# Performance work log

Measured on AMD Instinct MI355X. Metric: run time of the kernel, lower is better.

The kernel has to match this reference:

```python
import jax, jax.numpy as jnp
import numpy as np

EMB = 1024
HEADS = 16
HEAD_DIM = EMB // HEADS
B, S = 4, 2048


def setup_inputs() -> dict:
    key = jax.random.key(0)
    ks = jax.random.split(key, 9)
    sc = 1.0 / np.sqrt(EMB)
    x = jax.random.normal(ks[0], (B, S, EMB), dtype=jnp.float32)
    Wq = jax.random.normal(ks[1], (EMB, EMB), dtype=jnp.float32) * sc
    bq = jax.random.normal(ks[2], (EMB,), dtype=jnp.float32) * 0.02
    Wk = jax.random.normal(ks[3], (EMB, EMB), dtype=jnp.float32) * sc
    bk = jax.random.normal(ks[4], (EMB,), dtype=jnp.float32) * 0.02
    Wv = jax.random.normal(ks[5], (EMB, EMB), dtype=jnp.float32) * sc
    bv = jax.random.normal(ks[6], (EMB,), dtype=jnp.float32) * 0.02
    Wo = jax.random.normal(ks[7], (EMB, EMB), dtype=jnp.float32) * sc
    bo = jax.random.normal(ks[8], (EMB,), dtype=jnp.float32) * 0.02
    # causal mask: 1 where allowed (lower triangular), 0 elsewhere
    causal_mask = jnp.tril(jnp.ones((S, S), dtype=jnp.int32))[None, None]
    return {"x": x, "Wq": Wq, "bq": bq, "Wk": Wk, "bk": bk,
            "Wv": Wv, "bv": bv, "Wo": Wo, "bo": bo,
            "causal_mask": causal_mask}


def reference(x, Wq, bq, Wk, bk, Wv, bv, Wo, bo, causal_mask):
    bs, seq, _ = x.shape
    # nn.Linear: x @ W.T + b; then view [bs, seq, H, hd] and transpose to [bs, H, seq, hd]
    def proj(W, b):
        return (x @ W.T + b).reshape(bs, seq, HEADS, HEAD_DIM).transpose(0, 2, 1, 3)
    q, k, v = proj(Wq, bq), proj(Wk, bk), proj(Wv, bv)
    scale = 1.0 / np.sqrt(HEAD_DIM).astype(np.float32)
    dots = jnp.einsum('bhqd,bhkd->bhqk', q, k) * scale  # [B, H, S, S]
    dots = jnp.where(causal_mask == 0, -jnp.inf, dots)
    attn = jax.nn.softmax(dots, axis=-1)
    out = jnp.einsum('bhqk,bhkd->bhqd', attn, v)  # [B, H, S, hd]
    out = out.transpose(0, 2, 1, 3).reshape(bs, seq, EMB)
    return out @ Wo.T + bo
```

## Files before the change

### kernel.cpp

```cpp
#include <hip/hip_runtime.h>
#include <hip/hip_bf16.h>

typedef __attribute__((ext_vector_type(8))) short short8;
typedef __attribute__((ext_vector_type(4))) float floatx4;

#define B_    4
#define S_    2048
#define EMB_  1024
#define NH_   16
#define HD_   64

#if __has_builtin(__builtin_amdgcn_exp2f)
#define EXP2F(x) __builtin_amdgcn_exp2f(x)
#else
#define EXP2F(x) exp2f(x)
#endif

__device__ __forceinline__ void async_cp16(const void* g, void* l) {
  __builtin_amdgcn_global_load_lds(
      (const __attribute__((address_space(1))) unsigned int*)g,
      (__attribute__((address_space(3))) unsigned int*)l, 16, 0, 0);
}

__device__ __forceinline__ ushort4 cvt4(const float4 f) {
  __bf16 t[4] = {(__bf16)f.x, (__bf16)f.y, (__bf16)f.z, (__bf16)f.w};
  return *(const ushort4*)t;
}

__global__ __launch_bounds__(256)
void cvt_kernel(const float* __restrict__ x,
                const float* __restrict__ wq, const float* __restrict__ wk,
                const float* __restrict__ wv, const float* __restrict__ wo,
                const float* __restrict__ bq, const float* __restrict__ bk,
                const float* __restrict__ bv,
                __bf16* __restrict__ xb, __bf16* __restrict__ Wcat,
                __bf16* __restrict__ Wob, float* __restrict__ bcat)
{
  const int NX4 = 2097152;
  const int NW4 = 262144;
  int g = blockIdx.x * 256 + threadIdx.x;
  if (g < NX4) {
    *(ushort4*)(xb + (size_t)g * 4) = cvt4(*(const float4*)(x + (size_t)g * 4));
    return;
  }
  g -= NX4;
  if (g < 3 * NW4) {
    const float* src = (g < NW4) ? wq : (g < 2 * NW4) ? wk : wv;
    const int gg = (g < NW4) ? g : (g < 2 * NW4) ? g - NW4 : g - 2 * NW4;
    *(ushort4*)(Wcat + (size_t)g * 4) = cvt4(*(const float4*)(src + (size_t)gg * 4));
    return;
  }
  g -= 3 * NW4;
  if (g < NW4) {
    *(ushort4*)(Wob + (size_t)g * 4) = cvt4(*(const float4*)(wo + (size_t)g * 4));
    return;
  }
  g -= NW4;
  if (g < 768) {
    const float* src = (g < 256) ? bq : (g < 512) ? bk : bv;
    *(float4*)(bcat + (size_t)g * 4) = *(const float4*)(src + (size_t)(g & 255) * 4);
  }
}

__global__ __launch_bounds__(256)
void gemm_qkv_kernel(const __bf16* __restrict__ A, const __bf16* __restrict__ W,
                     const float* __restrict__ bcat,
                     __bf16* __restrict__ Qb, __bf16* __restrict__ Kb,
                     __bf16* __restrict__ Vb)
{
  __shared__ __attribute__((aligned(16))) __bf16 As[128 * 32];
  __shared__ __attribute__((aligned(16))) __bf16 Ws[128 * 32];
  const int tid  = threadIdx.x;
  const int wave = tid >> 6, lane = tid & 63;
  const int l15  = lane & 15, quad = lane >> 4;
  const int wm   = wave >> 1, wn = wave & 1;
  const int bm   = blockIdx.y * 128;
  const int bn   = blockIdx.x * 128;
  const int widx = bn >> 10;
  const float QS = 0.180336880f;

  floatx4 acc[4][4];
#pragma unroll
  for (int i = 0; i < 4; ++i)
#pragma unroll
    for (int j = 0; j < 4; ++j) acc[i][j] = (floatx4){0.f, 0.f, 0.f, 0.f};

  const int srow = tid >> 2;
  const int scol = (tid & 3) << 3;
  const __bf16* Ag = A + (size_t)(bm + srow) * 1024 + scol;
  const __bf16* Wg = W + (size_t)(bn + srow) * 1024 + scol;
  __bf16* AsD = As + tid * 8;
  __bf16* WsD = Ws + tid * 8;

  for (int k0 = 0; k0 < 1024; k0 += 32) {
    __syncthreads();
    async_cp16(Ag + k0,             AsD);
    async_cp16(Ag + k0 + 64 * 1024, AsD + 2048);
    async_cp16(Wg + k0,             WsD);
    async_cp16(Wg + k0 + 64 * 1024, WsD + 2048);
    __syncthreads();
    short8 af[4], wf[4];
#pragma unroll
    for (int mi = 0; mi < 4; ++mi)
      af[mi] = *(const short8*)(As + ((wm * 64 + mi * 16 + l15) << 5) + (quad << 3));
#pragma unroll
    for (int ni = 0; ni < 4; ++ni)
      wf[ni] = *(const short8*)(Ws + ((wn * 64 + ni * 16 + l15) << 5) + (quad << 3));
#pragma unroll
    for (int mi = 0; mi < 4; ++mi)
#pragma unroll
      for (int ni = 0; ni < 4; ++ni)
        acc[mi][ni] = __builtin_amdgcn_mfma_f32_16x16x32_bf16(af[mi], wf[ni], acc[mi][ni], 0, 0, 0);
  }

#pragma unroll
  for (int ni = 0; ni < 4; ++ni) {
    const int n  = bn + wn * 64 + ni * 16 + l15;
    const float bvb = bcat[n];
    const int np = n & 1023;
    const int h = np >> 6, d = np & 63;
#pragma unroll
    for (int mi = 0; mi < 4; ++mi) {
      const int m0 = bm + wm * 64 + mi * 16 + quad * 4;
      const int b = m0 >> 11, s0 = m0 & 2047;
      floatx4 v = acc[mi][ni];
      if (widx == 0) {
        const size_t base = (size_t)(b * 16 + h) * (S_ * 64) + d;
#pragma unroll
        for (int r = 0; r < 4; ++r)
          Qb[base + (size_t)(s0 + r) * 64] = (__bf16)((v[r] + bvb) * QS);
      } else if (widx == 1) {
        const size_t base = (size_t)(b * 16 + h) * (S_ * 64) + d;
#pragma unroll
        for (int r = 0; r < 4; ++r)
          Kb[base + (size_t)(s0 + r) * 64] = (__bf16)(v[r] + bvb);
      } else {
        const size_t base = ((size_t)(b * 16 + h) * 64 + d) * S_ + s0;
        union { ushort4 u4; unsigned short u[4]; } pk;
#pragma unroll
        for (int r = 0; r < 4; ++r) {
          __bf16 hv = (__bf16)(v[r] + bvb);
          pk.u[r] = *(unsigned short*)&hv;
        }
        *(ushort4*)(Vb + base) = pk.u4;
      }
    }
  }
}

__global__ __launch_bounds__(256, 4)
void attn_kernel(__bf16* __restrict__ Q, const __bf16* __restrict__ K,
                 const __bf16* __restrict__ Vt)
{
  __shared__ __attribute__((aligned(16))) __bf16 Ks[64 * 72];
  __shared__ __attribute__((aligned(16))) __bf16 Vs[64 * 72];
  __shared__ __attribute__((aligned(16))) __bf16 Ps[4][16 * 72];

  const int tid  = threadIdx.x;
  const int wave = tid >> 6, lane = tid & 63;
  const int l15  = lane & 15, quad = lane >> 4;
  const int qtA  = blockIdx.x, bh = blockIdx.y;
  const size_t hb = (size_t)bh * (S_ * 64);
  const float MASKV = -1.0e30f;

  const int srow = tid >> 3;
  const int scol = (tid & 7) << 3;

  for (int qsel = 0; qsel < 2; ++qsel) {
    const int qt = qsel ? (31 - qtA) : qtA;
    const int qw = qt * 64 + wave * 16;
    const int myq = qw + l15;

    short8 aq[2];
#pragma unroll
    for (int kk = 0; kk < 2; ++kk)
      aq[kk] = *(const short8*)(Q + hb + (size_t)myq * 64 + kk * 32 + quad * 8);

    floatx4 oacc[4];
#pragma unroll
    for (int j = 0; j < 4; ++j) oacc[j] = (floatx4){0.f, 0.f, 0.f, 0.f};
    float lsum = 0.0f;
    float mrun = MASKV;

    uint4 kreg0, kreg1, vreg0, vreg1;
    {
      const __bf16* kp = K  + hb + (size_t)srow * 64 + scol;
      const __bf16* vp = Vt + hb + (size_t)srow * S_ + scol;
      kreg0 = *(const uint4*)kp;
      kreg1 = *(const uint4*)(kp + 32 * 64);
      vreg0 = *(const uint4*)vp;
      vreg1 = *(const uint4*)(vp + (size_t)32 * S_);
    }

    for (int kt = 0; kt <= qt; ++kt) {
      __syncthreads();
      *(uint4*)(&Ks[srow * 72 + scol])        = kreg0;
      *(uint4*)(&Ks[(srow + 32) * 72 + scol]) = kreg1;
      *(uint4*)(&Vs[srow * 72 + scol])        = vreg0;
      *(uint4*)(&Vs[(srow + 32) * 72 + scol]) = vreg1;
      __syncthreads();

      if (kt < qt) {
        const __bf16* kp = K  + hb + (size_t)((kt + 1) * 64 + srow) * 64 + scol;
        const __bf16* vp = Vt + hb + (size_t)srow * S_ + (kt + 1) * 64 + scol;
        kreg0 = *(const uint4*)kp;
        kreg1 = *(const uint4*)(kp + 32 * 64);
        vreg0 = *(const uint4*)vp;
        vreg1 = *(const uint4*)(vp + (size_t)32 * S_);
      }

      floatx4 sacc[4];
#pragma unroll
      for (int j = 0; j < 4; ++j) sacc[j] = (floatx4){0.f, 0.f, 0.f, 0.f};
#pragma unroll
      for (int kk = 0; kk < 2; ++kk) {
        short8 bk[4];
#pragma unroll
        for (int ni = 0; ni < 4; ++ni)
          bk[ni] = *(const short8*)(&Ks[(ni * 16 + l15) * 72 + kk * 32 + quad * 8]);
#pragma unroll
        for (int ni = 0; ni < 4; ++ni)
          sacc[ni] = __builtin_amdgcn_mfma_f32_16x16x32_bf16(bk[ni], aq[kk], sacc[ni], 0, 0, 0);
      }

      if (kt == qt) {
        const int kb = kt * 64 + quad * 4;
#pragma unroll
        for (int ni = 0; ni < 4; ++ni)
#pragma unroll
          for (int r = 0; r < 4; ++r)
            if (kb + ni * 16 + r > myq) sacc[ni][r] = MASKV;
      }

      float t0 = fmaxf(fmaxf(sacc[0][0], sacc[0][1]), fmaxf(sacc[0][2], sacc[0][3]));
      float t1 = fmaxf(fmaxf(sacc[1][0], sacc[1][1]), fmaxf(sacc[1][2], sacc[1][3]));
      float t2 = fmaxf(fmaxf(sacc[2][0], sacc[2][1]), fmaxf(sacc[2][2], sacc[2][3]));
      float t3 = fmaxf(fmaxf(sacc[3][0], sacc[3][1]), fmaxf(sacc[3][2], sacc[3][3]));
      float tmax = fmaxf(fmaxf(t0, t1), fmaxf(t2, t3));
      tmax = fmaxf(tmax, __shfl_xor(tmax, 16));
      tmax = fmaxf(tmax, __shfl_xor(tmax, 32));

      const float mold = mrun;
      const float mnew = fmaxf(mold, tmax);
      mrun = mnew;
      const float alpha = EXP2F(mold - mnew);

      float psum = 0.0f;
#pragma unroll
      for (int ni = 0; ni < 4; ++ni) {
        float4 p;
        p.x = EXP2F(sacc[ni][0] - mnew);
        p.y = EXP2F(sacc[ni][1] - mnew);
        p.z = EXP2F(sacc[ni][2] - mnew);
        p.w = EXP2F(sacc[ni][3] - mnew);
        psum += (p.x + p.y) + (p.z + p.w);
        *(ushort4*)(&Ps[wave][l15 * 72 + ni * 16 + quad * 4]) = cvt4(p);
      }
      lsum = lsum * alpha + psum;
#pragma unroll
      for (int ni = 0; ni < 4; ++ni)
#pragma unroll
        for (int r = 0; r < 4; ++r) oacc[ni][r] *= alpha;

      asm volatile("s_waitcnt lgkmcnt(0)" ::: "memory");
      __builtin_amdgcn_sched_barrier(0);

#pragma unroll
      for (int kk = 0; kk < 2; ++kk) {
        const short8 pf = *(const short8*)(&Ps[wave][l15 * 72 + kk * 32 + quad * 8]);
        short8 bv[4];
#pragma unroll
        for (int ni = 0; ni < 4; ++ni)
          bv[ni] = *(const short8*)(&Vs[(ni * 16 + l15) * 72 + kk * 32 + quad * 8]);
#pragma unroll
        for (int ni = 0; ni < 4; ++ni)
          oacc[ni] = __builtin_amdgcn_mfma_f32_16x16x32_bf16(bv[ni], pf, oacc[ni], 0, 0, 0);
      }
    }

    float l = lsum;
    l += __shfl_xor(l, 16);
    l += __shfl_xor(l, 32);
    const float inv = 1.0f / fmaxf(l, 1e-20f);
    const size_t rowb = hb + (size_t)myq * 64;
#pragma unroll
    for (int ni = 0; ni < 4; ++ni) {
      float4 o;
      o.x = oacc[ni][0] * inv;
      o.y = oacc[ni][1] * inv;
      o.z = oacc[ni][2] * inv;
      o.w = oacc[ni][3] * inv;
      *(ushort4*)(Q + rowb + ni * 16 + quad * 4) = cvt4(o);
    }
  }
}

__global__ __launch_bounds__(256)
void gemm_o_kernel(const __bf16* __restrict__ A, const __bf16* __restrict__ W,
                   const float* __restrict__ bias, float* __restrict__ out)
{
  __shared__ __attribute__((aligned(16))) __bf16 As[128 * 32];
  __shared__ __attribute__((aligned(16))) __bf16 Ws[128 * 32];
  const int tid  = threadIdx.x;
  const int wave = tid >> 6, lane = tid & 63;
  const int l15  = lane & 15, quad = lane >> 4;
  const int wm   = wave >> 1, wn = wave & 1;
  const int bm   = blockIdx.y * 128;
  const int bn   = blockIdx.x * 128;

  floatx4 acc[4][4];
#pragma unroll
  for (int i = 0; i < 4; ++i)
#pragma unroll
    for (int j = 0; j < 4; ++j) acc[i][j] = (floatx4){0.f, 0.f, 0.f, 0.f};

  const int srow = tid >> 2;
  const int scol = (tid & 3) << 3;
  const __bf16* Wg = W + (size_t)(bn + srow) * 1024 + scol;
  const int bb = bm >> 11;
  const int ss = (bm & 2047) + srow;
  __bf16* AsD = As + tid * 8;
  __bf16* WsD = Ws + tid * 8;

  for (int k0 = 0; k0 < 1024; k0 += 32) {
    const int c = k0 + scol, h = c >> 6, dd = c & 63;
    const __bf16* pa0 = A + (((size_t)(bb * 16 + h) * S_) + ss) * 64 + dd;
    __syncthreads();
    async_cp16(pa0,           AsD);
    async_cp16(pa0 + 64 * 64, AsD + 2048);
    async_cp16(Wg + k0,             WsD);
    async_cp16(Wg + k0 + 64 * 1024, WsD + 2048);
    __syncthreads();

    short8 af[4], wf[4];
#pragma unroll
    for (int mi = 0; mi < 4; ++mi)
      af[mi] = *(const short8*)(As + ((wm * 64 + mi * 16 + l15) << 5) + (quad << 3));
#pragma unroll
    for (int ni = 0; ni < 4; ++ni)
      wf[ni] = *(const short8*)(Ws + ((wn * 64 + ni * 16 + l15) << 5) + (quad << 3));
#pragma unroll
    for (int mi = 0; mi < 4; ++mi)
#pragma unroll
      for (int ni = 0; ni < 4; ++ni)
        acc[mi][ni] = __builtin_amdgcn_mfma_f32_16x16x32_bf16(af[mi], wf[ni], acc[mi][ni], 0, 0, 0);
  }

#pragma unroll
  for (int ni = 0; ni < 4; ++ni) {
    const int n = bn + wn * 64 + ni * 16 + l15;
    const float bvb = bias[n];
#pragma unroll
    for (int mi = 0; mi < 4; ++mi) {
      const int m0 = bm + wm * 64 + mi * 16 + quad * 4;
      floatx4 v = acc[mi][ni];
#pragma unroll
      for (int r = 0; r < 4; ++r)
        out[(size_t)(m0 + r) * 1024 + n] = v[r] + bvb;
    }
  }
}

extern "C" void kernel_launch(void* const* d_in, const int* in_sizes, int n_in,
                              void* d_out, int out_size, void* d_ws, size_t ws_size,
                              hipStream_t stream) {
  const float* x  = (const float*)d_in[0];
  const float* Wq = (const float*)d_in[1];
  const float* bq = (const float*)d_in[2];
  const float* Wk = (const float*)d_in[3];
  const float* bk = (const float*)d_in[4];
  const float* Wv = (const float*)d_in[5];
  const float* bv = (const float*)d_in[6];
  const float* Wo = (const float*)d_in[7];
  const float* bo = (const float*)d_in[8];

  const size_t BUF = (size_t)B_ * NH_ * S_ * HD_;
  __bf16* ws   = (__bf16*)d_ws;
  __bf16* xb   = ws;
  __bf16* Wcat = ws + 8388608;
  __bf16* Wob  = ws + 11534336;
  __bf16* Qb   = ws + 12582912;
  float*  bcat = (float*)(ws + 20971520);
  __bf16* Kb   = (__bf16*)d_out;
  __bf16* Vb   = (__bf16*)d_out + BUF;

  dim3 blk(256);
  cvt_kernel<<<12291, blk, 0, stream>>>(x, Wq, Wk, Wv, Wo, bq, bk, bv,
                                        xb, Wcat, Wob, bcat);
  gemm_qkv_kernel<<<dim3(24, 64), blk, 0, stream>>>(xb, Wcat, bcat, Qb, Kb, Vb);
  attn_kernel<<<dim3(16, 64), blk, 0, stream>>>(Qb, Kb, Vb);
  gemm_o_kernel<<<dim3(8, 64), blk, 0, stream>>>(Qb, Wob, bo, (float*)d_out);
}
```

Measured before the change: 291.0 us.

## Process both paired query tiles in one KV sweep with lazy softmax rescale

Merges the two sequential query-tile passes (qtA and 31-qtA) into a single loop over key/value tiles. Each loaded K/V tile in LDS now serves both query tiles, which halves the global loads and barriers spent on the shared prefix. Softmax rescaling is skipped unless the running max grows by more than a threshold, which saves exp and multiply work on most iterations. The cost is double the accumulator registers, with the occupancy hint lowered from 4 to 3 blocks, and a per-wave Ps buffer for each query tile.

```diff
diff --git a/kernel.cpp b/kernel.cpp
--- a/kernel.cpp
+++ b/kernel.cpp
@@ -148,13 +148,51 @@
   }
 }
 
-__global__ __launch_bounds__(256, 4)
+__device__ __forceinline__ void softmax_update(
+    floatx4* s, float& mrun, float& lsum, floatx4* oacc,
+    __bf16* psbase, const int l15, const int quad)
+{
+  float t0 = fmaxf(fmaxf(s[0][0], s[0][1]), fmaxf(s[0][2], s[0][3]));
+  float t1 = fmaxf(fmaxf(s[1][0], s[1][1]), fmaxf(s[1][2], s[1][3]));
+  float t2 = fmaxf(fmaxf(s[2][0], s[2][1]), fmaxf(s[2][2], s[2][3]));
+  float t3 = fmaxf(fmaxf(s[3][0], s[3][1]), fmaxf(s[3][2], s[3][3]));
+  float tmax = fmaxf(fmaxf(t0, t1), fmaxf(t2, t3));
+  tmax = fmaxf(tmax, __shfl_xor(tmax, 16));
+  tmax = fmaxf(tmax, __shfl_xor(tmax, 32));
+
+  const float mold = mrun;
+  if (!__all(tmax <= mold + 8.0f)) {
+    const float mnew = fmaxf(mold, tmax);
+    const float alpha = EXP2F(mold - mnew);
+#pragma unroll
+    for (int ni = 0; ni < 4; ++ni)
+#pragma unroll
+      for (int r = 0; r < 4; ++r) oacc[ni][r] *= alpha;
+    lsum *= alpha;
+    mrun = mnew;
+  }
+  const float m = mrun;
+  float psum = 0.f;
+#pragma unroll
+  for (int ni = 0; ni < 4; ++ni) {
+    float4 p;
+    p.x = EXP2F(s[ni][0] - m);
+    p.y = EXP2F(s[ni][1] - m);
+    p.z = EXP2F(s[ni][2] - m);
+    p.w = EXP2F(s[ni][3] - m);
+    psum += (p.x + p.y) + (p.z + p.w);
+    *(ushort4*)(psbase + l15 * 72 + ni * 16 + quad * 4) = cvt4(p);
+  }
+  lsum += psum;
+}
+
+__global__ __launch_bounds__(256, 3)
 void attn_kernel(__bf16* __restrict__ Q, const __bf16* __restrict__ K,
                  const __bf16* __restrict__ Vt)
 {
   __shared__ __attribute__((aligned(16))) __bf16 Ks[64 * 72];
   __shared__ __attribute__((aligned(16))) __bf16 Vs[64 * 72];
-  __shared__ __attribute__((aligned(16))) __bf16 Ps[4][16 * 72];
+  __shared__ __attribute__((aligned(16))) __bf16 Ps[4][2][16 * 72];
 
   const int tid  = threadIdx.x;
   const int wave = tid >> 6, lane = tid & 63;
@@ -166,130 +204,150 @@
   const int srow = tid >> 3;
   const int scol = (tid & 7) << 3;
 
-  for (int qsel = 0; qsel < 2; ++qsel) {
-    const int qt = qsel ? (31 - qtA) : qtA;
-    const int qw = qt * 64 + wave * 16;
-    const int myq = qw + l15;
-
-    short8 aq[2];
-#pragma unroll
-    for (int kk = 0; kk < 2; ++kk)
-      aq[kk] = *(const short8*)(Q + hb + (size_t)myq * 64 + kk * 32 + quad * 8);
-
-    floatx4 oacc[4];
-#pragma unroll
-    for (int j = 0; j < 4; ++j) oacc[j] = (floatx4){0.f, 0.f, 0.f, 0.f};
-    float lsum = 0.0f;
-    float mrun = MASKV;
-
-    uint4 kreg0, kreg1, vreg0, vreg1;
-    {
-      const __bf16* kp = K  + hb + (size_t)srow * 64 + scol;
-      const __bf16* vp = Vt + hb + (size_t)srow * S_ + scol;
+  const int qtS = qtA;
+  const int qtB = 31 - qtA;
+  const int myqS = qtS * 64 + wave * 16 + l15;
+  const int myqB = qtB * 64 + wave * 16 + l15;
+
+  short8 aqS[2], aqB[2];
+#pragma unroll
+  for (int kk = 0; kk < 2; ++kk) {
+    aqS[kk] = *(const short8*)(Q + hb + (size_t)myqS * 64 + kk * 32 + quad * 8);
+    aqB[kk] = *(const short8*)(Q + hb + (size_t)myqB * 64 + kk * 32 + quad * 8);
+  }
+
+  floatx4 oaccS[4], oaccB[4];
+#pragma unroll
+  for (int j = 0; j < 4; ++j) {
+    oaccS[j] = (floatx4){0.f, 0.f, 0.f, 0.f};
+    oaccB[j] = (floatx4){0.f, 0.f, 0.f, 0.f};
+  }
+  float lsumS = 0.f, lsumB = 0.f;
+  float mrunS = MASKV, mrunB = MASKV;
+
+  uint4 kreg0, kreg1, vreg0, vreg1;
+  {
+    const __bf16* kp = K  + hb + (size_t)srow * 64 + scol;
+    const __bf16* vp = Vt + hb + (size_t)srow * S_ + scol;
+    kreg0 = *(const uint4*)kp;
+    kreg1 = *(const uint4*)(kp + 32 * 64);
+    vreg0 = *(const uint4*)vp;
+    vreg1 = *(const uint4*)(vp + (size_t)32 * S_);
+  }
+
+  for (int kt = 0; kt <= qtB; ++kt) {
+    const bool haveS = (kt <= qtS);
+
+    __syncthreads();
+    *(uint4*)(&Ks[srow * 72 + scol])        = kreg0;
+    *(uint4*)(&Ks[(srow + 32) * 72 + scol]) = kreg1;
+    *(uint4*)(&Vs[srow * 72 + scol])        = vreg0;
+    *(uint4*)(&Vs[(srow + 32) * 72 + scol]) = vreg1;
+    __syncthreads();
+
+    if (kt < qtB) {
+      const __bf16* kp = K  + hb + (size_t)((kt + 1) * 64 + srow) * 64 + scol;
+      const __bf16* vp = Vt + hb + (size_t)srow * S_ + (kt + 1) * 64 + scol;
       kreg0 = *(const uint4*)kp;
       kreg1 = *(const uint4*)(kp + 32 * 64);
       vreg0 = *(const uint4*)vp;
       vreg1 = *(const uint4*)(vp + (size_t)32 * S_);
     }
 
-    for (int kt = 0; kt <= qt; ++kt) {
-      __syncthreads();
-      *(uint4*)(&Ks[srow * 72 + scol])        = kreg0;
-      *(uint4*)(&Ks[(srow + 32) * 72 + scol]) = kreg1;
-      *(uint4*)(&Vs[srow * 72 + scol])        = vreg0;
-      *(uint4*)(&Vs[(srow + 32) * 72 + scol]) = vreg1;
-      __syncthreads();
-
-      if (kt < qt) {
-        const __bf16* kp = K  + hb + (size_t)((kt + 1) * 64 + srow) * 64 + scol;
-        const __bf16* vp = Vt + hb + (size_t)srow * S_ + (kt + 1) * 64 + scol;
-        kreg0 = *(const uint4*)kp;
-        kreg1 = *(const uint4*)(kp + 32 * 64);
-        vreg0 = *(const uint4*)vp;
-        vreg1 = *(const uint4*)(vp + (size_t)32 * S_);
+    floatx4 sS[4], sB[4];
+#pragma unroll
+    for (int j = 0; j < 4; ++j) {
+      sS[j] = (floatx4){0.f, 0.f, 0.f, 0.f};
+      sB[j] = (floatx4){0.f, 0.f, 0.f, 0.f};
+    }
+#pragma unroll
+    for (int kk = 0; kk < 2; ++kk) {
+      short8 bk[4];
+#pragma unroll
+      for (int ni = 0; ni < 4; ++ni)
+        bk[ni] = *(const short8*)(&Ks[(ni * 16 + l15) * 72 + kk * 32 + quad * 8]);
+#pragma unroll
+      for (int ni = 0; ni < 4; ++ni)
+        sB[ni] = __builtin_amdgcn_mfma_f32_16x16x32_bf16(bk[ni], aqB[kk], sB[ni], 0, 0, 0);
+      if (haveS) {
+#pragma unroll
+        for (int ni = 0; ni < 4; ++ni)
+          sS[ni] = __builtin_amdgcn_mfma_f32_16x16x32_bf16(bk[ni], aqS[kk], sS[ni], 0, 0, 0);
       }
-
-      floatx4 sacc[4];
-#pragma unroll
-      for (int j = 0; j < 4; ++j) sacc[j] = (floatx4){0.f, 0.f, 0.f, 0.f};
-#pragma unroll
-      for (int kk = 0; kk < 2; ++kk) {
-        short8 bk[4];
+    }
+
+    if (kt == qtB) {
+      const int kb = kt * 64 + quad * 4;
+#pragma unroll
+      for (int ni = 0; ni < 4; ++ni)
+#pragma unroll
+        for (int r = 0; r < 4; ++r)
+          if (kb + ni * 16 + r > myqB) sB[ni][r] = MASKV;
+    }
+    if (haveS) {
+      if (kt == qtS) {
+        const int kb = kt * 64 + quad * 4;
 #pragma unroll
         for (int ni = 0; ni < 4; ++ni)
-          bk[ni] = *(const short8*)(&Ks[(ni * 16 + l15) * 72 + kk * 32 + quad * 8]);
+#pragma unroll
+          for (int r = 0; r < 4; ++r)
+            if (kb + ni * 16 + r > myqS) sS[ni][r] = MASKV;
+      }
+      softmax_update(sS, mrunS, lsumS, oaccS, &Ps[wave][0][0], l15, quad);
+    }
+    softmax_update(sB, mrunB, lsumB, oaccB, &Ps[wave][1][0], l15, quad);
+
+    asm volatile("s_waitcnt lgkmcnt(0)" ::: "memory");
+    __builtin_amdgcn_sched_barrier(0);
+
+#pragma unroll
+    for (int kk = 0; kk < 2; ++kk) {
+      short8 bv[4];
+#pragma unroll
+      for (int ni = 0; ni < 4; ++ni)
+        bv[ni] = *(const short8*)(&Vs[(ni * 16 + l15) * 72 + kk * 32 + quad * 8]);
+      const short8 pfB = *(const short8*)(&Ps[wave][1][l15 * 72 + kk * 32 + quad * 8]);
+#pragma unroll
+      for (int ni = 0; ni < 4; ++ni)
+        oaccB[ni] = __builtin_amdgcn_mfma_f32_16x16x32_bf16(bv[ni], pfB, oaccB[ni], 0, 0, 0);
+      if (haveS) {
+        const short8 pfS = *(const short8*)(&Ps[wave][0][l15 * 72 + kk * 32 + quad * 8]);
 #pragma unroll
         for (int ni = 0; ni < 4; ++ni)
-          sacc[ni] = __builtin_amdgcn_mfma_f32_16x16x32_bf16(bk[ni], aq[kk], sacc[ni], 0, 0, 0);
+          oaccS[ni] = __builtin_amdgcn_mfma_f32_16x16x32_bf16(bv[ni], pfS, oaccS[ni], 0, 0, 0);
       }
-
-      if (kt == qt) {
-        const int kb = kt * 64 + quad * 4;
-#pragma unroll
-        for (int ni = 0; ni < 4; ++ni)
-#pragma unroll
-          for (int r = 0; r < 4; ++r)
-            if (kb + ni * 16 + r > myq) sacc[ni][r] = MASKV;
-      }
-
-      float t0 = fmaxf(fmaxf(sacc[0][0], sacc[0][1]), fmaxf(sacc[0][2], sacc[0][3]));
-      float t1 = fmaxf(fmaxf(sacc[1][0], sacc[1][1]), fmaxf(sacc[1][2], sacc[1][3]));
-      float t2 = fmaxf(fmaxf(sacc[2][0], sacc[2][1]), fmaxf(sacc[2][2], sacc[2][3]));
-      float t3 = fmaxf(fmaxf(sacc[3][0], sacc[3][1]), fmaxf(sacc[3][2], sacc[3][3]));
-      float tmax = fmaxf(fmaxf(t0, t1), fmaxf(t2, t3));
-      tmax = fmaxf(tmax, __shfl_xor(tmax, 16));
-      tmax = fmaxf(tmax, __shfl_xor(tmax, 32));
-
-      const float mold = mrun;
-      const float mnew = fmaxf(mold, tmax);
-      mrun = mnew;
-      const float alpha = EXP2F(mold - mnew);
-
-      float psum = 0.0f;
-#pragma unroll
-      for (int ni = 0; ni < 4; ++ni) {
-        float4 p;
-        p.x = EXP2F(sacc[ni][0] - mnew);
-        p.y = EXP2F(sacc[ni][1] - mnew);
-        p.z = EXP2F(sacc[ni][2] - mnew);
-        p.w = EXP2F(sacc[ni][3] - mnew);
-        psum += (p.x + p.y) + (p.z + p.w);
-        *(ushort4*)(&Ps[wave][l15 * 72 + ni * 16 + quad * 4]) = cvt4(p);
-      }
-      lsum = lsum * alpha + psum;
-#pragma unroll
-      for (int ni = 0; ni < 4; ++ni)
-#pragma unroll
-        for (int r = 0; r < 4; ++r) oacc[ni][r] *= alpha;
-
-      asm volatile("s_waitcnt lgkmcnt(0)" ::: "memory");
-      __builtin_amdgcn_sched_barrier(0);
-
-#pragma unroll
-      for (int kk = 0; kk < 2; ++kk) {
-        const short8 pf = *(const short8*)(&Ps[wave][l15 * 72 + kk * 32 + quad * 8]);
-        short8 bv[4];
-#pragma unroll
-        for (int ni = 0; ni < 4; ++ni)
-          bv[ni] = *(const short8*)(&Vs[(ni * 16 + l15) * 72 + kk * 32 + quad * 8]);
-#pragma unroll
-        for (int ni = 0; ni < 4; ++ni)
-          oacc[ni] = __builtin_amdgcn_mfma_f32_16x16x32_bf16(bv[ni], pf, oacc[ni], 0, 0, 0);
-      }
-    }
-
-    float l = lsum;
+    }
+  }
+
+  {
+    float l = lsumS;
     l += __shfl_xor(l, 16);
     l += __shfl_xor(l, 32);
     const float inv = 1.0f / fmaxf(l, 1e-20f);
-    const size_t rowb = hb + (size_t)myq * 64;
+    const size_t rowb = hb + (size_t)myqS * 64;
 #pragma unroll
     for (int ni = 0; ni < 4; ++ni) {
       float4 o;
-      o.x = oacc[ni][0] * inv;
-      o.y = oacc[ni][1] * inv;
-      o.z = oacc[ni][2] * inv;
-      o.w = oacc[ni][3] * inv;
+      o.x = oaccS[ni][0] * inv;
+      o.y = oaccS[ni][1] * inv;
+      o.z = oaccS[ni][2] * inv;
+      o.w = oaccS[ni][3] * inv;
+      *(ushort4*)(Q + rowb + ni * 16 + quad * 4) = cvt4(o);
+    }
+  }
+  {
+    float l = lsumB;
+    l += __shfl_xor(l, 16);
+    l += __shfl_xor(l, 32);
+    const float inv = 1.0f / fmaxf(l, 1e-20f);
+    const size_t rowb = hb + (size_t)myqB * 64;
+#pragma unroll
+    for (int ni = 0; ni < 4; ++ni) {
+      float4 o;
+      o.x = oaccB[ni][0] * inv;
+      o.y = oaccB[ni][1] * inv;
+      o.z = oaccB[ni][2] * inv;
+      o.w = oaccB[ni][3] * inv;
       *(ushort4*)(Q + rowb + ni * 16 + quad * 4) = cvt4(o);
     }
   }
```

Result: no change. 287.2 us (-1.3%).

## Switch attention to 32x32x16 MFMA with two 32-row waves and lazy rescale

Applied to the files above, without the earlier changes.

The attention kernel now runs two waves of 32 query rows each (128 threads) and uses 32x32x16 bf16 MFMAs instead of 16x16x32, which reduces LDS fragment reads per FLOP and cross-lane reductions. The K/V staging is reworked so each thread loads four contiguous 16-byte chunks. The online-softmax rescale is skipped unless some lane's tile max exceeds the running max by more than 8 (in log2 units), which saves exp and multiply work per tile but lets unnormalised values grow by up to 2^8. Fewer threads per block may lower latency hiding, since each block now has half as many waves.

```diff
diff --git a/kernel.cpp b/kernel.cpp
--- a/kernel.cpp
+++ b/kernel.cpp
@@ -3,6 +3,7 @@
 
 typedef __attribute__((ext_vector_type(8))) short short8;
 typedef __attribute__((ext_vector_type(4))) float floatx4;
+typedef __attribute__((ext_vector_type(16))) float floatx16;
 
 #define B_    4
 #define S_    2048
@@ -148,150 +149,156 @@
   }
 }
 
-__global__ __launch_bounds__(256, 4)
+__global__ __launch_bounds__(128, 2)
 void attn_kernel(__bf16* __restrict__ Q, const __bf16* __restrict__ K,
                  const __bf16* __restrict__ Vt)
 {
   __shared__ __attribute__((aligned(16))) __bf16 Ks[64 * 72];
   __shared__ __attribute__((aligned(16))) __bf16 Vs[64 * 72];
-  __shared__ __attribute__((aligned(16))) __bf16 Ps[4][16 * 72];
+  __shared__ __attribute__((aligned(16))) __bf16 Ps[2][32 * 72];
 
   const int tid  = threadIdx.x;
   const int wave = tid >> 6, lane = tid & 63;
-  const int l15  = lane & 15, quad = lane >> 4;
+  const int l31  = lane & 31, h = lane >> 5;
   const int qtA  = blockIdx.x, bh = blockIdx.y;
   const size_t hb = (size_t)bh * (S_ * 64);
   const float MASKV = -1.0e30f;
 
-  const int srow = tid >> 3;
-  const int scol = (tid & 7) << 3;
+  const int srow = tid >> 1;
+  const int scol = (tid & 1) << 5;
 
   for (int qsel = 0; qsel < 2; ++qsel) {
     const int qt = qsel ? (31 - qtA) : qtA;
-    const int qw = qt * 64 + wave * 16;
-    const int myq = qw + l15;
-
-    short8 aq[2];
-#pragma unroll
-    for (int kk = 0; kk < 2; ++kk)
-      aq[kk] = *(const short8*)(Q + hb + (size_t)myq * 64 + kk * 32 + quad * 8);
-
-    floatx4 oacc[4];
-#pragma unroll
-    for (int j = 0; j < 4; ++j) oacc[j] = (floatx4){0.f, 0.f, 0.f, 0.f};
+    const int myq = qt * 64 + wave * 32 + l31;
+
+    short8 aq[4];
+#pragma unroll
+    for (int s = 0; s < 4; ++s)
+      aq[s] = *(const short8*)(Q + hb + (size_t)myq * 64 + s * 16 + h * 8);
+
+    floatx16 oacc[2];
+#pragma unroll
+    for (int dt = 0; dt < 2; ++dt)
+#pragma unroll
+      for (int r = 0; r < 16; ++r) oacc[dt][r] = 0.f;
     float lsum = 0.0f;
     float mrun = MASKV;
 
-    uint4 kreg0, kreg1, vreg0, vreg1;
+    uint4 kreg[4], vreg[4];
     {
       const __bf16* kp = K  + hb + (size_t)srow * 64 + scol;
       const __bf16* vp = Vt + hb + (size_t)srow * S_ + scol;
-      kreg0 = *(const uint4*)kp;
-      kreg1 = *(const uint4*)(kp + 32 * 64);
-      vreg0 = *(const uint4*)vp;
-      vreg1 = *(const uint4*)(vp + (size_t)32 * S_);
+#pragma unroll
+      for (int u = 0; u < 4; ++u) {
+        kreg[u] = *(const uint4*)(kp + u * 8);
+        vreg[u] = *(const uint4*)(vp + u * 8);
+      }
     }
 
     for (int kt = 0; kt <= qt; ++kt) {
       __syncthreads();
-      *(uint4*)(&Ks[srow * 72 + scol])        = kreg0;
-      *(uint4*)(&Ks[(srow + 32) * 72 + scol]) = kreg1;
-      *(uint4*)(&Vs[srow * 72 + scol])        = vreg0;
-      *(uint4*)(&Vs[(srow + 32) * 72 + scol]) = vreg1;
+#pragma unroll
+      for (int u = 0; u < 4; ++u) {
+        *(uint4*)(&Ks[srow * 72 + scol + u * 8]) = kreg[u];
+        *(uint4*)(&Vs[srow * 72 + scol + u * 8]) = vreg[u];
+      }
       __syncthreads();
 
       if (kt < qt) {
         const __bf16* kp = K  + hb + (size_t)((kt + 1) * 64 + srow) * 64 + scol;
         const __bf16* vp = Vt + hb + (size_t)srow * S_ + (kt + 1) * 64 + scol;
-        kreg0 = *(const uint4*)kp;
-        kreg1 = *(const uint4*)(kp + 32 * 64);
-        vreg0 = *(const uint4*)vp;
-        vreg1 = *(const uint4*)(vp + (size_t)32 * S_);
-      }
-
-      floatx4 sacc[4];
-#pragma unroll
-      for (int j = 0; j < 4; ++j) sacc[j] = (floatx4){0.f, 0.f, 0.f, 0.f};
-#pragma unroll
-      for (int kk = 0; kk < 2; ++kk) {
-        short8 bk[4];
-#pragma unroll
-        for (int ni = 0; ni < 4; ++ni)
-          bk[ni] = *(const short8*)(&Ks[(ni * 16 + l15) * 72 + kk * 32 + quad * 8]);
-#pragma unroll
-        for (int ni = 0; ni < 4; ++ni)
-          sacc[ni] = __builtin_amdgcn_mfma_f32_16x16x32_bf16(bk[ni], aq[kk], sacc[ni], 0, 0, 0);
+#pragma unroll
+        for (int u = 0; u < 4; ++u) {
+          kreg[u] = *(const uint4*)(kp + u * 8);
+          vreg[u] = *(const uint4*)(vp + u * 8);
+        }
+      }
+
+      floatx16 sacc[2];
+#pragma unroll
+      for (int sub = 0; sub < 2; ++sub)
+#pragma unroll
+        for (int r = 0; r < 16; ++r) sacc[sub][r] = 0.f;
+#pragma unroll
+      for (int s = 0; s < 4; ++s) {
+        short8 ak0 = *(const short8*)(&Ks[(l31)      * 72 + s * 16 + h * 8]);
+        short8 ak1 = *(const short8*)(&Ks[(32 + l31) * 72 + s * 16 + h * 8]);
+        sacc[0] = __builtin_amdgcn_mfma_f32_32x32x16_bf16(ak0, aq[s], sacc[0], 0, 0, 0);
+        sacc[1] = __builtin_amdgcn_mfma_f32_32x32x16_bf16(ak1, aq[s], sacc[1], 0, 0, 0);
       }
 
       if (kt == qt) {
-        const int kb = kt * 64 + quad * 4;
-#pragma unroll
-        for (int ni = 0; ni < 4; ++ni)
-#pragma unroll
-          for (int r = 0; r < 4; ++r)
-            if (kb + ni * 16 + r > myq) sacc[ni][r] = MASKV;
-      }
-
-      float t0 = fmaxf(fmaxf(sacc[0][0], sacc[0][1]), fmaxf(sacc[0][2], sacc[0][3]));
-      float t1 = fmaxf(fmaxf(sacc[1][0], sacc[1][1]), fmaxf(sacc[1][2], sacc[1][3]));
-      float t2 = fmaxf(fmaxf(sacc[2][0], sacc[2][1]), fmaxf(sacc[2][2], sacc[2][3]));
-      float t3 = fmaxf(fmaxf(sacc[3][0], sacc[3][1]), fmaxf(sacc[3][2], sacc[3][3]));
-      float tmax = fmaxf(fmaxf(t0, t1), fmaxf(t2, t3));
-      tmax = fmaxf(tmax, __shfl_xor(tmax, 16));
+#pragma unroll
+        for (int sub = 0; sub < 2; ++sub)
+#pragma unroll
+          for (int r = 0; r < 16; ++r) {
+            const int kg = kt * 64 + sub * 32 + (r & 3) + 8 * (r >> 2) + 4 * h;
+            if (kg > myq) sacc[sub][r] = MASKV;
+          }
+      }
+
+      float tmax = MASKV;
+#pragma unroll
+      for (int sub = 0; sub < 2; ++sub)
+#pragma unroll
+        for (int r = 0; r < 16; ++r) tmax = fmaxf(tmax, sacc[sub][r]);
       tmax = fmaxf(tmax, __shfl_xor(tmax, 32));
 
       const float mold = mrun;
-      const float mnew = fmaxf(mold, tmax);
-      mrun = mnew;
-      const float alpha = EXP2F(mold - mnew);
-
-      float psum = 0.0f;
-#pragma unroll
-      for (int ni = 0; ni < 4; ++ni) {
-        float4 p;
-        p.x = EXP2F(sacc[ni][0] - mnew);
-        p.y = EXP2F(sacc[ni][1] - mnew);
-        p.z = EXP2F(sacc[ni][2] - mnew);
-        p.w = EXP2F(sacc[ni][3] - mnew);
-        psum += (p.x + p.y) + (p.z + p.w);
-        *(ushort4*)(&Ps[wave][l15 * 72 + ni * 16 + quad * 4]) = cvt4(p);
-      }
-      lsum = lsum * alpha + psum;
-#pragma unroll
-      for (int ni = 0; ni < 4; ++ni)
-#pragma unroll
-        for (int r = 0; r < 4; ++r) oacc[ni][r] *= alpha;
+      if (!__all(tmax <= mold + 8.0f)) {
+        const float mnew = fmaxf(mold, tmax);
+        const float alpha = EXP2F(mold - mnew);
+#pragma unroll
+        for (int dt = 0; dt < 2; ++dt)
+#pragma unroll
+          for (int r = 0; r < 16; ++r) oacc[dt][r] *= alpha;
+        lsum *= alpha;
+        mrun = mnew;
+      }
+      const float m = mrun;
+
+      float psum = 0.f;
+#pragma unroll
+      for (int sub = 0; sub < 2; ++sub)
+#pragma unroll
+        for (int m4 = 0; m4 < 4; ++m4) {
+          float4 p;
+          p.x = EXP2F(sacc[sub][4 * m4 + 0] - m);
+          p.y = EXP2F(sacc[sub][4 * m4 + 1] - m);
+          p.z = EXP2F(sacc[sub][4 * m4 + 2] - m);
+          p.w = EXP2F(sacc[sub][4 * m4 + 3] - m);
+          psum += (p.x + p.y) + (p.z + p.w);
+          *(ushort4*)(&Ps[wave][l31 * 72 + sub * 32 + 8 * m4 + 4 * h]) = cvt4(p);
+        }
+      lsum += psum;
 
       asm volatile("s_waitcnt lgkmcnt(0)" ::: "memory");
       __builtin_amdgcn_sched_barrier(0);
 
 #pragma unroll
-      for (int kk = 0; kk < 2; ++kk) {
-        const short8 pf = *(const short8*)(&Ps[wave][l15 * 72 + kk * 32 + quad * 8]);
-        short8 bv[4];
-#pragma unroll
-        for (int ni = 0; ni < 4; ++ni)
-          bv[ni] = *(const short8*)(&Vs[(ni * 16 + l15) * 72 + kk * 32 + quad * 8]);
-#pragma unroll
-        for (int ni = 0; ni < 4; ++ni)
-          oacc[ni] = __builtin_amdgcn_mfma_f32_16x16x32_bf16(bv[ni], pf, oacc[ni], 0, 0, 0);
+      for (int st = 0; st < 4; ++st) {
+        const short8 pf = *(const short8*)(&Ps[wave][l31 * 72 + st * 16 + h * 8]);
+        short8 av0 = *(const short8*)(&Vs[(l31)      * 72 + st * 16 + h * 8]);
+        short8 av1 = *(const short8*)(&Vs[(32 + l31) * 72 + st * 16 + h * 8]);
+        oacc[0] = __builtin_amdgcn_mfma_f32_32x32x16_bf16(av0, pf, oacc[0], 0, 0, 0);
+        oacc[1] = __builtin_amdgcn_mfma_f32_32x32x16_bf16(av1, pf, oacc[1], 0, 0, 0);
       }
     }
 
-    float l = lsum;
-    l += __shfl_xor(l, 16);
-    l += __shfl_xor(l, 32);
+    float l = lsum + __shfl_xor(lsum, 32);
     const float inv = 1.0f / fmaxf(l, 1e-20f);
     const size_t rowb = hb + (size_t)myq * 64;
 #pragma unroll
-    for (int ni = 0; ni < 4; ++ni) {
-      float4 o;
-      o.x = oacc[ni][0] * inv;
-      o.y = oacc[ni][1] * inv;
-      o.z = oacc[ni][2] * inv;
-      o.w = oacc[ni][3] * inv;
-      *(ushort4*)(Q + rowb + ni * 16 + quad * 4) = cvt4(o);
-    }
+    for (int dt = 0; dt < 2; ++dt)
+#pragma unroll
+      for (int m4 = 0; m4 < 4; ++m4) {
+        float4 o;
+        o.x = oacc[dt][4 * m4 + 0] * inv;
+        o.y = oacc[dt][4 * m4 + 1] * inv;
+        o.z = oacc[dt][4 * m4 + 2] * inv;
+        o.w = oacc[dt][4 * m4 + 3] * inv;
+        *(ushort4*)(Q + rowb + dt * 32 + 8 * m4 + 4 * h) = cvt4(o);
+      }
   }
 }
 
@@ -323,8 +330,8 @@
   __bf16* WsD = Ws + tid * 8;
 
   for (int k0 = 0; k0 < 1024; k0 += 32) {
-    const int c = k0 + scol, h = c >> 6, dd = c & 63;
-    const __bf16* pa0 = A + (((size_t)(bb * 16 + h) * S_) + ss) * 64 + dd;
+    const int c = k0 + scol, hh = c >> 6, dd = c & 63;
+    const __bf16* pa0 = A + (((size_t)(bb * 16 + hh) * S_) + ss) * 64 + dd;
     __syncthreads();
     async_cp16(pa0,           AsD);
     async_cp16(pa0 + 64 * 64, AsD + 2048);
@@ -384,10 +391,9 @@
   __bf16* Kb   = (__bf16*)d_out;
   __bf16* Vb   = (__bf16*)d_out + BUF;
 
-  dim3 blk(256);
-  cvt_kernel<<<12291, blk, 0, stream>>>(x, Wq, Wk, Wv, Wo, bq, bk, bv,
-                                        xb, Wcat, Wob, bcat);
-  gemm_qkv_kernel<<<dim3(24, 64), blk, 0, stream>>>(xb, Wcat, bcat, Qb, Kb, Vb);
-  attn_kernel<<<dim3(16, 64), blk, 0, stream>>>(Qb, Kb, Vb);
-  gemm_o_kernel<<<dim3(8, 64), blk, 0, stream>>>(Qb, Wob, bo, (float*)d_out);
-}
+  cvt_kernel<<<12291, dim3(256), 0, stream>>>(x, Wq, Wk, Wv, Wo, bq, bk, bv,
+                                              xb, Wcat, Wob, bcat);
+  gemm_qkv_kernel<<<dim3(24, 64), dim3(256), 0, stream>>>(xb, Wcat, bcat, Qb, Kb, Vb);
+  attn_kernel<<<dim3(16, 64), dim3(128), 0, stream>>>(Qb, Kb, Vb);
+  gemm_o_kernel<<<dim3(8, 64), dim3(256), 0, stream>>>(Qb, Wob, bo, (float*)d_out);
+}
```

After: 387.9 us. +33.3%, slower.

## Stage 128-key tiles per barrier pair and skip rescale when max grows little

Applied to the files above, without the earlier changes.

The attention loop now loads 128 keys of K and V per iteration into larger shared buffers and processes them as two 64-key subtiles. This halves the number of __syncthreads pairs and global-load rounds per query tile. It also adds a lazy online-softmax rescale: the accumulators are rescaled only when some lane's running max grows by more than 8 in the log2 domain. The cost is more shared memory and registers, so occupancy drops from 4 to 3 blocks per CU. The lazy threshold also lets unnormalised exponentials grow up to 2^8, which could affect precision.

```diff
diff --git a/kernel.cpp b/kernel.cpp
--- a/kernel.cpp
+++ b/kernel.cpp
@@ -148,12 +148,12 @@
   }
 }
 
-__global__ __launch_bounds__(256, 4)
+__global__ __launch_bounds__(256, 3)
 void attn_kernel(__bf16* __restrict__ Q, const __bf16* __restrict__ K,
                  const __bf16* __restrict__ Vt)
 {
-  __shared__ __attribute__((aligned(16))) __bf16 Ks[64 * 72];
-  __shared__ __attribute__((aligned(16))) __bf16 Vs[64 * 72];
+  __shared__ __attribute__((aligned(16))) __bf16 Ks[128 * 72];
+  __shared__ __attribute__((aligned(16))) __bf16 Vs[64 * 136];
   __shared__ __attribute__((aligned(16))) __bf16 Ps[4][16 * 72];
 
   const int tid  = threadIdx.x;
@@ -165,11 +165,14 @@
 
   const int srow = tid >> 3;
   const int scol = (tid & 7) << 3;
+  const int vrow = tid >> 2;
+  const int vcol = (tid & 3) << 5;
 
   for (int qsel = 0; qsel < 2; ++qsel) {
     const int qt = qsel ? (31 - qtA) : qtA;
     const int qw = qt * 64 + wave * 16;
     const int myq = qw + l15;
+    const int nkt = (qt >> 1) + 1;
 
     short8 aq[2];
 #pragma unroll
@@ -182,99 +185,112 @@
     float lsum = 0.0f;
     float mrun = MASKV;
 
-    uint4 kreg0, kreg1, vreg0, vreg1;
+    uint4 kreg[4], vreg[4];
     {
       const __bf16* kp = K  + hb + (size_t)srow * 64 + scol;
-      const __bf16* vp = Vt + hb + (size_t)srow * S_ + scol;
-      kreg0 = *(const uint4*)kp;
-      kreg1 = *(const uint4*)(kp + 32 * 64);
-      vreg0 = *(const uint4*)vp;
-      vreg1 = *(const uint4*)(vp + (size_t)32 * S_);
+      const __bf16* vp = Vt + hb + (size_t)vrow * S_ + vcol;
+#pragma unroll
+      for (int u = 0; u < 4; ++u) {
+        kreg[u] = *(const uint4*)(kp + (size_t)u * 32 * 64);
+        vreg[u] = *(const uint4*)(vp + u * 8);
+      }
     }
 
-    for (int kt = 0; kt <= qt; ++kt) {
+    for (int ktt = 0; ktt < nkt; ++ktt) {
       __syncthreads();
-      *(uint4*)(&Ks[srow * 72 + scol])        = kreg0;
-      *(uint4*)(&Ks[(srow + 32) * 72 + scol]) = kreg1;
-      *(uint4*)(&Vs[srow * 72 + scol])        = vreg0;
-      *(uint4*)(&Vs[(srow + 32) * 72 + scol]) = vreg1;
+#pragma unroll
+      for (int u = 0; u < 4; ++u) {
+        *(uint4*)(&Ks[(srow + u * 32) * 72 + scol]) = kreg[u];
+        *(uint4*)(&Vs[vrow * 136 + vcol + u * 8])   = vreg[u];
+      }
       __syncthreads();
 
-      if (kt < qt) {
-        const __bf16* kp = K  + hb + (size_t)((kt + 1) * 64 + srow) * 64 + scol;
-        const __bf16* vp = Vt + hb + (size_t)srow * S_ + (kt + 1) * 64 + scol;
-        kreg0 = *(const uint4*)kp;
-        kreg1 = *(const uint4*)(kp + 32 * 64);
-        vreg0 = *(const uint4*)vp;
-        vreg1 = *(const uint4*)(vp + (size_t)32 * S_);
+      if (ktt + 1 < nkt) {
+        const __bf16* kp = K  + hb + (size_t)((ktt + 1) * 128 + srow) * 64 + scol;
+        const __bf16* vp = Vt + hb + (size_t)vrow * S_ + (ktt + 1) * 128 + vcol;
+#pragma unroll
+        for (int u = 0; u < 4; ++u) {
+          kreg[u] = *(const uint4*)(kp + (size_t)u * 32 * 64);
+          vreg[u] = *(const uint4*)(vp + u * 8);
+        }
       }
 
-      floatx4 sacc[4];
-#pragma unroll
-      for (int j = 0; j < 4; ++j) sacc[j] = (floatx4){0.f, 0.f, 0.f, 0.f};
-#pragma unroll
-      for (int kk = 0; kk < 2; ++kk) {
-        short8 bk[4];
-#pragma unroll
-        for (int ni = 0; ni < 4; ++ni)
-          bk[ni] = *(const short8*)(&Ks[(ni * 16 + l15) * 72 + kk * 32 + quad * 8]);
-#pragma unroll
-        for (int ni = 0; ni < 4; ++ni)
-          sacc[ni] = __builtin_amdgcn_mfma_f32_16x16x32_bf16(bk[ni], aq[kk], sacc[ni], 0, 0, 0);
-      }
-
-      if (kt == qt) {
-        const int kb = kt * 64 + quad * 4;
-#pragma unroll
-        for (int ni = 0; ni < 4; ++ni)
-#pragma unroll
-          for (int r = 0; r < 4; ++r)
-            if (kb + ni * 16 + r > myq) sacc[ni][r] = MASKV;
-      }
-
-      float t0 = fmaxf(fmaxf(sacc[0][0], sacc[0][1]), fmaxf(sacc[0][2], sacc[0][3]));
-      float t1 = fmaxf(fmaxf(sacc[1][0], sacc[1][1]), fmaxf(sacc[1][2], sacc[1][3]));
-      float t2 = fmaxf(fmaxf(sacc[2][0], sacc[2][1]), fmaxf(sacc[2][2], sacc[2][3]));
-      float t3 = fmaxf(fmaxf(sacc[3][0], sacc[3][1]), fmaxf(sacc[3][2], sacc[3][3]));
-      float tmax = fmaxf(fmaxf(t0, t1), fmaxf(t2, t3));
-      tmax = fmaxf(tmax, __shfl_xor(tmax, 16));
-      tmax = fmaxf(tmax, __shfl_xor(tmax, 32));
-
-      const float mold = mrun;
-      const float mnew = fmaxf(mold, tmax);
-      mrun = mnew;
-      const float alpha = EXP2F(mold - mnew);
-
-      float psum = 0.0f;
-#pragma unroll
-      for (int ni = 0; ni < 4; ++ni) {
-        float4 p;
-        p.x = EXP2F(sacc[ni][0] - mnew);
-        p.y = EXP2F(sacc[ni][1] - mnew);
-        p.z = EXP2F(sacc[ni][2] - mnew);
-        p.w = EXP2F(sacc[ni][3] - mnew);
-        psum += (p.x + p.y) + (p.z + p.w);
-        *(ushort4*)(&Ps[wave][l15 * 72 + ni * 16 + quad * 4]) = cvt4(p);
-      }
-      lsum = lsum * alpha + psum;
-#pragma unroll
-      for (int ni = 0; ni < 4; ++ni)
-#pragma unroll
-        for (int r = 0; r < 4; ++r) oacc[ni][r] *= alpha;
-
-      asm volatile("s_waitcnt lgkmcnt(0)" ::: "memory");
-      __builtin_amdgcn_sched_barrier(0);
-
-#pragma unroll
-      for (int kk = 0; kk < 2; ++kk) {
-        const short8 pf = *(const short8*)(&Ps[wave][l15 * 72 + kk * 32 + quad * 8]);
-        short8 bv[4];
-#pragma unroll
-        for (int ni = 0; ni < 4; ++ni)
-          bv[ni] = *(const short8*)(&Vs[(ni * 16 + l15) * 72 + kk * 32 + quad * 8]);
-#pragma unroll
-        for (int ni = 0; ni < 4; ++ni)
-          oacc[ni] = __builtin_amdgcn_mfma_f32_16x16x32_bf16(bv[ni], pf, oacc[ni], 0, 0, 0);
+#pragma unroll
+      for (int s2 = 0; s2 < 2; ++s2) {
+        const int ksub = ktt * 2 + s2;
+        if (ksub <= qt) {
+          floatx4 sacc[4];
+#pragma unroll
+          for (int j = 0; j < 4; ++j) sacc[j] = (floatx4){0.f, 0.f, 0.f, 0.f};
+#pragma unroll
+          for (int kk = 0; kk < 2; ++kk) {
+            short8 bk[4];
+#pragma unroll
+            for (int ni = 0; ni < 4; ++ni)
+              bk[ni] = *(const short8*)(&Ks[(s2 * 64 + ni * 16 + l15) * 72 + kk * 32 + quad * 8]);
+#pragma unroll
+            for (int ni = 0; ni < 4; ++ni)
+              sacc[ni] = __builtin_amdgcn_mfma_f32_16x16x32_bf16(bk[ni], aq[kk], sacc[ni], 0, 0, 0);
+          }
+
+          if (ksub == qt) {
+            const int kb = ksub * 64 + quad * 4;
+#pragma unroll
+            for (int ni = 0; ni < 4; ++ni)
+#pragma unroll
+              for (int r = 0; r < 4; ++r)
+                if (kb + ni * 16 + r > myq) sacc[ni][r] = MASKV;
+          }
+
+          float t0 = fmaxf(fmaxf(sacc[0][0], sacc[0][1]), fmaxf(sacc[0][2], sacc[0][3]));
+          float t1 = fmaxf(fmaxf(sacc[1][0], sacc[1][1]), fmaxf(sacc[1][2], sacc[1][3]));
+          float t2 = fmaxf(fmaxf(sacc[2][0], sacc[2][1]), fmaxf(sacc[2][2], sacc[2][3]));
+          float t3 = fmaxf(fmaxf(sacc[3][0], sacc[3][1]), fmaxf(sacc[3][2], sacc[3][3]));
+          float tmax = fmaxf(fmaxf(t0, t1), fmaxf(t2, t3));
+          tmax = fmaxf(tmax, __shfl_xor(tmax, 16));
+          tmax = fmaxf(tmax, __shfl_xor(tmax, 32));
+
+          const float mold = mrun;
+          if (!__all(tmax <= mold + 8.0f)) {
+            const float mnew = fmaxf(mold, tmax);
+            const float alpha = EXP2F(mold - mnew);
+#pragma unroll
+            for (int ni = 0; ni < 4; ++ni)
+#pragma unroll
+              for (int r = 0; r < 4; ++r) oacc[ni][r] *= alpha;
+            lsum *= alpha;
+            mrun = mnew;
+          }
+          const float m = mrun;
+
+          float psum = 0.f;
+#pragma unroll
+          for (int ni = 0; ni < 4; ++ni) {
+            float4 p;
+            p.x = EXP2F(sacc[ni][0] - m);
+            p.y = EXP2F(sacc[ni][1] - m);
+            p.z = EXP2F(sacc[ni][2] - m);
+            p.w = EXP2F(sacc[ni][3] - m);
+            psum += (p.x + p.y) + (p.z + p.w);
+            *(ushort4*)(&Ps[wave][l15 * 72 + ni * 16 + quad * 4]) = cvt4(p);
+          }
+          lsum += psum;
+
+          asm volatile("s_waitcnt lgkmcnt(0)" ::: "memory");
+          __builtin_amdgcn_sched_barrier(0);
+
+#pragma unroll
+          for (int kk = 0; kk < 2; ++kk) {
+            const short8 pf = *(const short8*)(&Ps[wave][l15 * 72 + kk * 32 + quad * 8]);
+            short8 bv[4];
+#pragma unroll
+            for (int ni = 0; ni < 4; ++ni)
+              bv[ni] = *(const short8*)(&Vs[(ni * 16 + l15) * 136 + s2 * 64 + kk * 32 + quad * 8]);
+#pragma unroll
+            for (int ni = 0; ni < 4; ++ni)
+              oacc[ni] = __builtin_amdgcn_mfma_f32_16x16x32_bf16(bv[ni], pf, oacc[ni], 0, 0, 0);
+          }
+        }
       }
     }
 
```

After: 417.1 us. 1.43x slower.
